# Optimization experiments

Hardware: AMD Instinct MI355X
Metric: run time of the kernel (lower is better)

The kernel has to match this reference:

```python
import jax, jax.numpy as jnp
import numpy as np


def setup_inputs() -> dict:
    key = jax.random.key(0)
    ks = jax.random.split(key, 7)
    C = 512
    x = jax.random.normal(ks[0], (16, C, 64, 64), dtype=jnp.float32)
    wq = jax.random.normal(ks[1], (C, C), dtype=jnp.float32) * (1.0 / np.sqrt(C))
    bq = jax.random.normal(ks[2], (C,), dtype=jnp.float32) * 0.02
    wk = jax.random.normal(ks[3], (C, C), dtype=jnp.float32) * (1.0 / np.sqrt(C))
    bk = jax.random.normal(ks[4], (C,), dtype=jnp.float32) * 0.02
    wo = jax.random.normal(ks[5], (C, C), dtype=jnp.float32) * (1.0 / np.sqrt(C))
    bo = jax.random.normal(ks[6], (C,), dtype=jnp.float32) * 0.02
    return {"x": x, "wq": wq, "bq": bq, "wk": wk, "bk": bk, "wo": wo, "bo": bo, "num_heads": 8}


def _conv1x1(x, w, b):
    # 1x1 conv == per-pixel linear map over channels; w: [Cout, Cin]
    return jnp.einsum('oc,bchw->bohw', w, x) + b[None, :, None, None]


def reference(x, wq, bq, wk, bk, wo, bo, num_heads):
    B, C, H, W = x.shape
    dh = C // num_heads
    P = H * W  # spatial positions (tokens)
    q = _conv1x1(x, wq, bq).reshape(B, num_heads, dh, P)
    k = _conv1x1(x, wk, bk).reshape(B, num_heads, dh, P)
    v = x.reshape(B, num_heads, dh, P)
    # NOTE: faithful to the torch code, attention is [B, nh, dh, dh]
    # (channel-channel scores contracted over spatial positions).
    att = jnp.einsum('bndp,bnep->bnde', q, k) / jnp.sqrt(jnp.asarray(dh, x.dtype))
    att = jax.nn.softmax(att, axis=-1)
    out = jnp.einsum('bnde,bnep->bndp', att, v).reshape(B, C, H, W)
    out = _conv1x1(out, wo, bo)
    return out + x
```

## Files before the change

### kernel.cpp

```cpp
#include <hip/hip_runtime.h>


typedef unsigned short ushort_t;
typedef __attribute__((ext_vector_type(8))) short bf16x8;
typedef __attribute__((ext_vector_type(4))) float f32x4;
typedef __attribute__((ext_vector_type(4))) unsigned short us4;
typedef __attribute__((ext_vector_type(8))) unsigned short us8;

#define NB 16
#define NC 512
#define NP 4096
#define NHD 8
#define DH 64

#define BM 128
#define BN 128
#define BKK 64

__device__ inline ushort_t f2bf(float f) {
  unsigned int u = __float_as_uint(f);
  u += 0x7FFFu + ((u >> 16) & 1u);
  return (ushort_t)(u >> 16);
}
__device__ inline float bf2f(ushort_t h) {
  return __uint_as_float(((unsigned int)h) << 16);
}

__device__ inline void gld_lds16(const void* g, void* l) {
  __builtin_amdgcn_global_load_lds(
      (const __attribute__((address_space(1))) unsigned int*)g,
      (__attribute__((address_space(3))) unsigned int*)l, 16, 0, 0);
}

__global__ __launch_bounds__(256, 4) void k_mfma_bt(
    const ushort_t* __restrict__ A, const ushort_t* __restrict__ B,
    void* __restrict__ Cv, const float* __restrict__ bias,
    int lda, int ldb, int ldc, long long sA, long long sB, long long sC,
    int Kper, int mode, int flags) {
  __shared__ __align__(128) ushort_t As[BM * BKK];
  __shared__ __align__(128) ushort_t Bs[BN * BKK];
  int m0, n0;
  long long zc;
  const ushort_t *Ab, *Bb;
  if (flags & 2) {
    int flat = blockIdx.x + 10 * blockIdx.z;
    int nf = (flat & 7) * 80 + (flat >> 3);
    int z2 = nf / 10, tile = nf - z2 * 10;
    int bb = z2 >> 2, sp = z2 & 3;
    int tm = (0x1A449000u >> (tile * 3)) & 7;
    int tn = (0x1B4D1688u >> (tile * 3)) & 7;
    m0 = tm * BM; n0 = tn * BN;
    Ab = A + bb * sA + (long long)sp * Kper;
    Bb = B + bb * sB + (long long)sp * Kper;
    zc = (long long)z2 * sC;
  } else {
    int bx = blockIdx.x, by = blockIdx.y;
    if (flags & 1) {
      int nxy = gridDim.x * gridDim.y;
      int id = bx + gridDim.x * by;
      int nid = (id & 7) * (nxy >> 3) + (id >> 3);
      bx = nid % gridDim.x; by = nid / gridDim.x;
    }
    m0 = by * BM; n0 = bx * BN;
    Ab = A + blockIdx.z * sA;
    Bb = B + blockIdx.z * sB;
    zc = (long long)blockIdx.z * sC;
  }
  int t = threadIdx.x;
  int lane = t & 63, w = t >> 6;
  int wr = w >> 1, wc = w & 1;
  int l15 = lane & 15, l4 = lane >> 4;
  int sr = lane >> 3, scc = lane & 7;

  f32x4 zero = {0.f, 0.f, 0.f, 0.f};
  f32x4 acc[4][4];
#pragma unroll
  for (int i = 0; i < 4; ++i)
#pragma unroll
    for (int j = 0; j < 4; ++j) acc[i][j] = zero;

  for (int k0 = 0; k0 < Kper; k0 += BKK) {
#pragma unroll
    for (int i = 0; i < 4; ++i) {
      int slab = w * 4 + i;
      int r = slab * 8 + sr;
      int kc = scc ^ (r & 7);
      gld_lds16(Ab + (size_t)(m0 + r) * lda + k0 + kc * 8, &As[slab * 512]);
      gld_lds16(Bb + (size_t)(n0 + r) * ldb + k0 + kc * 8, &Bs[slab * 512]);
    }
    __syncthreads();
#pragma unroll
    for (int kf = 0; kf < 2; ++kf) {
      bf16x8 av[4], bv[4];
#pragma unroll
      for (int i = 0; i < 4; ++i) {
        int r = wr * 64 + i * 16 + l15;
        int c = (kf * 4 + l4) ^ (r & 7);
        av[i] = *(const bf16x8*)&As[r * 64 + c * 8];
        int rn = wc * 64 + i * 16 + l15;
        int cn = (kf * 4 + l4) ^ (rn & 7);
        bv[i] = *(const bf16x8*)&Bs[rn * 64 + cn * 8];
      }
#pragma unroll
      for (int i = 0; i < 4; ++i)
#pragma unroll
        for (int j = 0; j < 4; ++j)
          acc[i][j] = __builtin_amdgcn_mfma_f32_16x16x32_bf16(av[i], bv[j],
                                                              acc[i][j], 0, 0, 0);
    }
    __syncthreads();
  }

  if (mode == 3) {
    ushort_t* C = (ushort_t*)Cv + zc;
#pragma unroll
    for (int i = 0; i < 4; ++i)
#pragma unroll
      for (int j = 0; j < 4; ++j)
#pragma unroll
        for (int rr = 0; rr < 4; ++rr) {
          int grow = m0 + wr * 64 + i * 16 + l4 * 4 + rr;
          int gcol = n0 + wc * 64 + j * 16 + l15;
          float v = acc[i][j][rr];
          ushort_t hi = f2bf(v);
          C[(size_t)grow * ldc + gcol] = hi;
          C[4194304 + (size_t)grow * ldc + gcol] = f2bf(v - bf2f(hi));
        }
  } else if (mode == 1) {
    float* C = (float*)Cv + zc;
#pragma unroll
    for (int i = 0; i < 4; ++i)
#pragma unroll
      for (int j = 0; j < 4; ++j)
#pragma unroll
        for (int rr = 0; rr < 4; ++rr) {
          int grow = m0 + wr * 64 + i * 16 + l4 * 4 + rr;
          int gcol = n0 + wc * 64 + j * 16 + l15;
          __builtin_nontemporal_store(acc[i][j][rr] + bias[grow],
                                      &C[(size_t)grow * ldc + gcol]);
        }
  } else {
    float* C = (float*)Cv + zc;
#pragma unroll
    for (int i = 0; i < 4; ++i)
#pragma unroll
      for (int j = 0; j < 4; ++j)
#pragma unroll
        for (int rr = 0; rr < 4; ++rr) {
          int grow = m0 + wr * 64 + i * 16 + l4 * 4 + rr;
          int gcol = n0 + wc * 64 + j * 16 + l15;
          C[(size_t)grow * ldc + gcol] = acc[i][j][rr];
        }
  }
}

__global__ __launch_bounds__(256) void k_prep(const float* __restrict__ x,
                                              ushort_t* __restrict__ xbf,
                                              ushort_t* __restrict__ xt,
                                              float* __restrict__ sPart) {
  __shared__ float tile[64][65];
  int b = blockIdx.z;
  const float* xb = x + (size_t)b * NC * NP;
  int t = threadIdx.x;
  int pp0 = blockIdx.x * 64, cc0 = blockIdx.y * 64;
#pragma unroll
  for (int i = 0; i < 4; ++i) {
    int idx = i * 256 + t;
    int r = idx >> 4, q = idx & 15;
    float4 v = *reinterpret_cast<const float4*>(
        xb + (size_t)(cc0 + r) * NP + pp0 + q * 4);
    us4 u = {f2bf(v.x), f2bf(v.y), f2bf(v.z), f2bf(v.w)};
    *reinterpret_cast<us4*>(
        &xbf[((size_t)b * NC + cc0 + r) * NP + pp0 + q * 4]) = u;
    tile[r][q * 4 + 0] = v.x; tile[r][q * 4 + 1] = v.y;
    tile[r][q * 4 + 2] = v.z; tile[r][q * 4 + 3] = v.w;
  }
  __syncthreads();
  {
    int r = t >> 2, q = t & 3;
    float ps = 0.f;
#pragma unroll
    for (int i = 0; i < 16; ++i) ps += tile[r][q * 16 + i];
    ps += __shfl_down(ps, 1, 64);
    ps += __shfl_down(ps, 2, 64);
    if (q == 0)
      sPart[(size_t)blockIdx.x * (NB * NC) + b * NC + cc0 + r] = ps;
  }
  {
    int p = t >> 2, cg = t & 3;
    us8 lo, hi;
#pragma unroll
    for (int i = 0; i < 8; ++i) lo[i] = f2bf(tile[cg * 16 + i][p]);
#pragma unroll
    for (int i = 0; i < 8; ++i) hi[i] = f2bf(tile[cg * 16 + 8 + i][p]);
    ushort_t* dst = &xt[((size_t)b * NP + pp0 + p) * NC + cc0 + cg * 16];
    *reinterpret_cast<us8*>(dst) = lo;
    *reinterpret_cast<us8*>(dst + 8) = hi;
  }
}

__global__ __launch_bounds__(256) void k_sreduce(const float* __restrict__ sPart,
                                                 float* __restrict__ s) {
  int idx = blockIdx.x * 256 + threadIdx.x;
  float a = 0.f;
  for (int pb = 0; pb < 64; ++pb) a += sPart[(size_t)pb * (NB * NC) + idx];
  s[idx] = a;
}

__global__ __launch_bounds__(256) void k_cvtw(
    const float* __restrict__ wq, const float* __restrict__ wk,
    const float* __restrict__ wo, ushort_t* __restrict__ q,
    ushort_t* __restrict__ k, ushort_t* __restrict__ o) {
  int i = blockIdx.x * 256 + threadIdx.x;
  q[i] = f2bf(wq[i]);
  k[i] = f2bf(wk[i]);
  o[i] = f2bf(wo[i]);
}

__global__ __launch_bounds__(256) void k_reduceG(const float* __restrict__ Gp,
                                                 ushort_t* __restrict__ Gb) {
  size_t i = (size_t)blockIdx.x * 256 + threadIdx.x;
  size_t b = i >> 18, idx = i & 262143;
  int r = (int)(idx >> 9), c = (int)(idx & 511);
  int rr = r, cc = c;
  if ((r >> 7) > (c >> 7)) { rr = c; cc = r; }
  const float* p = Gp + (b * 4) * 262144 + (size_t)rr * 512 + cc;
  float v = (p[0] + p[262144]) + (p[2 * 262144] + p[3 * 262144]);
  Gb[i] = f2bf(v);
}

__global__ __launch_bounds__(256) void k_uw(
    const float* __restrict__ wq, const float* __restrict__ wk,
    const float* __restrict__ s, float* __restrict__ U, float* __restrict__ W) {
  int b = blockIdx.x >> 3, n = blockIdx.x & 7;
  int t = threadIdx.x;
  __shared__ float ssh[NC];
  for (int i = t; i < NC; i += 256) ssh[i] = s[b * NC + i];
  __syncthreads();
  int pair = t >> 1, half = t & 1;
  int d = pair & 63, sel = pair >> 6;
  const float* row = (sel ? wk : wq) + (size_t)(n * DH + d) * NC + half * 256;
  const float* sb = ssh + half * 256;
  float a = 0.f;
#pragma unroll 8
  for (int i = 0; i < 64; ++i) {
    float4 v = reinterpret_cast<const float4*>(row)[i];
    a += v.x * sb[i * 4] + v.y * sb[i * 4 + 1] + v.z * sb[i * 4 + 2] +
         v.w * sb[i * 4 + 3];
  }
  a += __shfl_xor(a, 1, 64);
  if (half == 0) (sel ? W : U)[b * NC + n * DH + d] = a;
}

__global__ __launch_bounds__(256) void k_fused(
    const ushort_t* __restrict__ Thi, const ushort_t* __restrict__ Tlo,
    const ushort_t* __restrict__ Wkb, const ushort_t* __restrict__ Wob,
    const float* __restrict__ U, const float* __restrict__ Wv,
    const float* __restrict__ bq, const float* __restrict__ bk,
    ushort_t* __restrict__ Mb) {
  __shared__ __align__(128) ushort_t Th[64 * 64];
  __shared__ __align__(128) ushort_t Tl[64 * 64];
  __shared__ __align__(128) ushort_t Wks[64 * 64];
  __shared__ float Ps[64][65];
  __shared__ __align__(16) ushort_t PT[64 * 72];
  __shared__ __align__(128) ushort_t Wos[128 * 64];
  __shared__ float ush[64], wsh[64], bqs[64], bks[64];

  int b = blockIdx.x >> 4, n = (blockIdx.x >> 1) & 7, half = blockIdx.x & 1;
  int t = threadIdx.x, lane = t & 63, w = t >> 6;
  int l15 = lane & 15, l4 = lane >> 4;

  if (t < 64) ush[t] = U[b * NC + n * DH + t];
  else if (t < 128) wsh[t - 64] = Wv[b * NC + n * DH + (t - 64)];
  else if (t < 192) bqs[t - 128] = bq[n * DH + (t - 128)];
  else bks[t - 192] = bk[n * DH + (t - 192)];

  const size_t tbase = ((size_t)b * NC + n * DH) * NC;
  f32x4 zero = {0.f, 0.f, 0.f, 0.f};
  f32x4 acc[4];
#pragma unroll
  for (int i = 0; i < 4; ++i) acc[i] = zero;

  for (int kc0 = 0; kc0 < NC; kc0 += 64) {
    __syncthreads();
#pragma unroll
    for (int i = 0; i < 6; ++i) {
      int slab = w * 6 + i;
      int mat = slab >> 3, sl = slab & 7;
      int r = sl * 8 + (lane >> 3);
      int kc = (lane & 7) ^ (r & 7);
      if (mat == 0)
        gld_lds16(Thi + tbase + (size_t)r * NC + kc0 + kc * 8, &Th[sl * 512]);
      else if (mat == 1)
        gld_lds16(Tlo + tbase + (size_t)r * NC + kc0 + kc * 8, &Tl[sl * 512]);
      else
        gld_lds16(Wkb + (size_t)(n * DH + r) * NC + kc0 + kc * 8, &Wks[sl * 512]);
    }
    __syncthreads();
#pragma unroll
    for (int kf = 0; kf < 2; ++kf) {
      int rn = w * 16 + l15;
      int cn = (kf * 4 + l4) ^ (rn & 7);
      bf16x8 bvf = *(const bf16x8*)&Wks[rn * 64 + cn * 8];
#pragma unroll
      for (int i = 0; i < 4; ++i) {
        int r = i * 16 + l15;
        int c = (kf * 4 + l4) ^ (r & 7);
        bf16x8 ah = *(const bf16x8*)&Th[r * 64 + c * 8];
        bf16x8 al = *(const bf16x8*)&Tl[r * 64 + c * 8];
        acc[i] = __builtin_amdgcn_mfma_f32_16x16x32_bf16(ah, bvf, acc[i], 0, 0, 0);
        acc[i] = __builtin_amdgcn_mfma_f32_16x16x32_bf16(al, bvf, acc[i], 0, 0, 0);
      }
    }
  }
#pragma unroll
  for (int i = 0; i < 4; ++i)
#pragma unroll
    for (int rr = 0; rr < 4; ++rr) {
      int d = i * 16 + l4 * 4 + rr, e = w * 16 + l15;
      float v = acc[i][rr] + ush[d] * bks[e] + bqs[d] * (wsh[e] + 4096.f * bks[e]);
      Ps[d][e] = v * 0.125f;
    }
  __syncthreads();
  {
    int d = w * 16 + l15;
    float mx = -1e30f;
#pragma unroll
    for (int i = 0; i < 16; ++i) mx = fmaxf(mx, Ps[d][l4 * 16 + i]);
    mx = fmaxf(mx, __shfl_xor(mx, 16, 64));
    mx = fmaxf(mx, __shfl_xor(mx, 32, 64));
    float pv[16];
    float sum = 0.f;
#pragma unroll
    for (int i = 0; i < 16; ++i) {
      pv[i] = __expf(Ps[d][l4 * 16 + i] - mx);
      sum += pv[i];
    }
    sum += __shfl_xor(sum, 16, 64);
    sum += __shfl_xor(sum, 32, 64);
    float inv = 1.f / sum;
#pragma unroll
    for (int i = 0; i < 16; ++i) PT[(l4 * 16 + i) * 72 + d] = f2bf(pv[i] * inv);
  }
  for (int mi = 0; mi < 2; ++mi) {
    int mt = half * 2 + mi;
    __syncthreads();
#pragma unroll
    for (int i = 0; i < 4; ++i) {
      int slab = w * 4 + i;
      int r = slab * 8 + (lane >> 3);
      int kc = (lane & 7) ^ (r & 7);
      gld_lds16(Wob + (size_t)(mt * 128 + r) * NC + n * DH + kc * 8,
                &Wos[slab * 512]);
    }
    __syncthreads();
    f32x4 acc2[2][4];
#pragma unroll
    for (int i2 = 0; i2 < 2; ++i2)
#pragma unroll
      for (int j = 0; j < 4; ++j) acc2[i2][j] = zero;
#pragma unroll
    for (int kf = 0; kf < 2; ++kf) {
      bf16x8 bv[4];
#pragma unroll
      for (int j = 0; j < 4; ++j) {
        int e = j * 16 + l15;
        bv[j] = *(const bf16x8*)&PT[e * 72 + (kf * 4 + l4) * 8];
      }
#pragma unroll
      for (int i2 = 0; i2 < 2; ++i2) {
        int r = w * 32 + i2 * 16 + l15;
        int c = (kf * 4 + l4) ^ (r & 7);
        bf16x8 av = *(const bf16x8*)&Wos[r * 64 + c * 8];
#pragma unroll
        for (int j = 0; j < 4; ++j)
          acc2[i2][j] =
              __builtin_amdgcn_mfma_f32_16x16x32_bf16(av, bv[j], acc2[i2][j], 0, 0, 0);
      }
    }
#pragma unroll
    for (int i2 = 0; i2 < 2; ++i2)
#pragma unroll
      for (int j = 0; j < 4; ++j)
#pragma unroll
        for (int rr = 0; rr < 4; ++rr) {
          int grow = mt * 128 + w * 32 + i2 * 16 + l4 * 4 + rr;
          int gcol = n * DH + j * 16 + l15;
          float v = acc2[i2][j][rr];
          if (grow == gcol) v += 1.f;
          Mb[((size_t)b * NC + grow) * NC + gcol] = f2bf(v);
        }
  }
}

#define BKt 32
#define BMt 128
#define BNt 128
#define LDTK 132

__global__ __launch_bounds__(256) void k_rowsum(const float* __restrict__ x,
                                                float* __restrict__ s) {
  int row = blockIdx.x;
  const float* xr = x + (size_t)row * NP;
  int t = threadIdx.x;
  float acc = 0.f;
  for (int i = t; i < NP / 4; i += 256) {
    float4 v = reinterpret_cast<const float4*>(xr)[i];
    acc += (v.x + v.y) + (v.z + v.w);
  }
  for (int off = 32; off > 0; off >>= 1) acc += __shfl_down(acc, off, 64);
  __shared__ float red[4];
  int lane = t & 63, wv = t >> 6;
  if (lane == 0) red[wv] = acc;
  __syncthreads();
  if (t == 0) s[row] = (red[0] + red[1]) + (red[2] + red[3]);
}

__global__ __launch_bounds__(256) void k_gemm_abT(
    const float* __restrict__ Abase, const float* __restrict__ Bbase,
    float* __restrict__ Cbase, int K, int lda, int ldb, int ldc,
    size_t sA, size_t sB, size_t sC) {
  __shared__ float As[BKt][LDTK];
  __shared__ float Bs[BKt][LDTK];
  const float* A = Abase + sA * blockIdx.z;
  const float* Bm = Bbase + sB * blockIdx.z;
  float* Cm = Cbase + sC * blockIdx.z;
  int m0 = blockIdx.y * BMt, n0 = blockIdx.x * BNt;
  int t = threadIdx.x;
  int tr = t >> 4, tc = t & 15;
  float acc[8][8];
#pragma unroll
  for (int i = 0; i < 8; ++i)
#pragma unroll
    for (int j = 0; j < 8; ++j) acc[i][j] = 0.f;
  for (int k0 = 0; k0 < K; k0 += BKt) {
#pragma unroll
    for (int it = 0; it < 4; ++it) {
      int idx = it * 256 + t;
      int r = idx >> 3, kq = idx & 7;
      float4 va = *reinterpret_cast<const float4*>(A + (size_t)(m0 + r) * lda + k0 + kq * 4);
      As[kq * 4 + 0][r] = va.x; As[kq * 4 + 1][r] = va.y;
      As[kq * 4 + 2][r] = va.z; As[kq * 4 + 3][r] = va.w;
      float4 vb = *reinterpret_cast<const float4*>(Bm + (size_t)(n0 + r) * ldb + k0 + kq * 4);
      Bs[kq * 4 + 0][r] = vb.x; Bs[kq * 4 + 1][r] = vb.y;
      Bs[kq * 4 + 2][r] = vb.z; Bs[kq * 4 + 3][r] = vb.w;
    }
    __syncthreads();
#pragma unroll
    for (int kk = 0; kk < BKt; ++kk) {
      float4 a0 = *reinterpret_cast<const float4*>(&As[kk][tr * 8]);
      float4 a1 = *reinterpret_cast<const float4*>(&As[kk][tr * 8 + 4]);
      float4 b0 = *reinterpret_cast<const float4*>(&Bs[kk][tc * 8]);
      float4 b1 = *reinterpret_cast<const float4*>(&Bs[kk][tc * 8 + 4]);
      float av[8] = {a0.x, a0.y, a0.z, a0.w, a1.x, a1.y, a1.z, a1.w};
      float bv[8] = {b0.x, b0.y, b0.z, b0.w, b1.x, b1.y, b1.z, b1.w};
#pragma unroll
      for (int i = 0; i < 8; ++i)
#pragma unroll
        for (int j = 0; j < 8; ++j) acc[i][j] += av[i] * bv[j];
    }
    __syncthreads();
  }
#pragma unroll
  for (int i = 0; i < 8; ++i) {
    float* crow = Cm + (size_t)(m0 + tr * 8 + i) * ldc + n0 + tc * 8;
    float4 c0 = {acc[i][0], acc[i][1], acc[i][2], acc[i][3]};
    float4 c1 = {acc[i][4], acc[i][5], acc[i][6], acc[i][7]};
    *reinterpret_cast<float4*>(crow) = c0;
    *reinterpret_cast<float4*>(crow + 4) = c1;
  }
}

__global__ __launch_bounds__(256) void k_gemm_ab(
    const float* __restrict__ Abase, const float* __restrict__ Bbase,
    float* __restrict__ Cbase, const float* __restrict__ bias,
    int K, int lda, int ldb, int ldc, size_t sA, size_t sB, size_t sC) {
  __shared__ float As[BKt][LDTK];
  __shared__ float Bs[BKt][LDTK];
  const float* A = Abase + sA * blockIdx.z;
  const float* Bm = Bbase + sB * blockIdx.z;
  float* Cm = Cbase + sC * blockIdx.z;
  int m0 = blockIdx.y * BMt, n0 = blockIdx.x * BNt;
  int t = threadIdx.x;
  int tr = t >> 4, tc = t & 15;
  float acc[8][8];
#pragma unroll
  for (int i = 0; i < 8; ++i)
#pragma unroll
    for (int j = 0; j < 8; ++j) acc[i][j] = 0.f;
  for (int k0 = 0; k0 < K; k0 += BKt) {
#pragma unroll
    for (int it = 0; it < 4; ++it) {
      int idx = it * 256 + t;
      int r = idx >> 3, kq = idx & 7;
      float4 va = *reinterpret_cast<const float4*>(A + (size_t)(m0 + r) * lda + k0 + kq * 4);
      As[kq * 4 + 0][r] = va.x; As[kq * 4 + 1][r] = va.y;
      As[kq * 4 + 2][r] = va.z; As[kq * 4 + 3][r] = va.w;
      int kk = idx >> 5, nq = idx & 31;
      float4 vb = *reinterpret_cast<const float4*>(Bm + (size_t)(k0 + kk) * ldb + n0 + nq * 4);
      *reinterpret_cast<float4*>(&Bs[kk][nq * 4]) = vb;
    }
    __syncthreads();
#pragma unroll
    for (int kk = 0; kk < BKt; ++kk) {
      float4 a0 = *reinterpret_cast<const float4*>(&As[kk][tr * 8]);
      float4 a1 = *reinterpret_cast<const float4*>(&As[kk][tr * 8 + 4]);
      float4 b0 = *reinterpret_cast<const float4*>(&Bs[kk][tc * 8]);
      float4 b1 = *reinterpret_cast<const float4*>(&Bs[kk][tc * 8 + 4]);
      float av[8] = {a0.x, a0.y, a0.z, a0.w, a1.x, a1.y, a1.z, a1.w};
      float bv[8] = {b0.x, b0.y, b0.z, b0.w, b1.x, b1.y, b1.z, b1.w};
#pragma unroll
      for (int i = 0; i < 8; ++i)
#pragma unroll
        for (int j = 0; j < 8; ++j) acc[i][j] += av[i] * bv[j];
    }
    __syncthreads();
  }
#pragma unroll
  for (int i = 0; i < 8; ++i) {
    int row = m0 + tr * 8 + i;
    float bb = bias ? bias[row] : 0.f;
    float* crow = Cm + (size_t)row * ldc + n0 + tc * 8;
    float4 c0 = {acc[i][0] + bb, acc[i][1] + bb, acc[i][2] + bb, acc[i][3] + bb};
    float4 c1 = {acc[i][4] + bb, acc[i][5] + bb, acc[i][6] + bb, acc[i][7] + bb};
    *reinterpret_cast<float4*>(crow) = c0;
    *reinterpret_cast<float4*>(crow + 4) = c1;
  }
}

__global__ __launch_bounds__(256) void k_att(
    const float* __restrict__ T, const float* __restrict__ wq,
    const float* __restrict__ bq, const float* __restrict__ wk,
    const float* __restrict__ bk, const float* __restrict__ wo,
    const float* __restrict__ s, float* __restrict__ Mf) {
  int b = blockIdx.x >> 3, n = blockIdx.x & 7;
  int t = threadIdx.x;
  __shared__ float sh_s[NC];
  __shared__ float sh_u[DH], sh_w[DH];
  __shared__ float L[DH][DH + 1];
  __shared__ float Ts[DH][68];
  __shared__ float Ks[DH][68];

  for (int i = t; i < NC; i += 256) sh_s[i] = s[b * NC + i];
  __syncthreads();
  if (t < 128) {
    int d = t & 63;
    const float* wrow = (t < 64 ? wq : wk) + (size_t)(n * DH + d) * NC;
    float a = 0.f;
    for (int c = 0; c < NC; ++c) a += wrow[c] * sh_s[c];
    if (t < 64) sh_u[d] = a; else sh_w[d] = a;
  }

  int d = t >> 2, eg = t & 3;
  float acc[16];
#pragma unroll
  for (int i = 0; i < 16; ++i) acc[i] = 0.f;

  for (int c0 = 0; c0 < NC; c0 += 64) {
#pragma unroll
    for (int it = 0; it < 4; ++it) {
      int idx = it * 256 + t;
      int r = idx >> 4, cq = idx & 15;
      float4 v = *reinterpret_cast<const float4*>(
          T + ((size_t)b * NC + n * DH + r) * NC + c0 + cq * 4);
      *reinterpret_cast<float4*>(&Ts[r][cq * 4]) = v;
      float4 kv = *reinterpret_cast<const float4*>(
          wk + (size_t)(n * DH + r) * NC + c0 + cq * 4);
      Ks[cq * 4 + 0][r] = kv.x; Ks[cq * 4 + 1][r] = kv.y;
      Ks[cq * 4 + 2][r] = kv.z; Ks[cq * 4 + 3][r] = kv.w;
    }
    __syncthreads();
    for (int cc = 0; cc < 64; ++cc) {
      float tv = Ts[d][cc];
      float4 k0v = *reinterpret_cast<const float4*>(&Ks[cc][eg * 16]);
      float4 k1v = *reinterpret_cast<const float4*>(&Ks[cc][eg * 16 + 4]);
      float4 k2v = *reinterpret_cast<const float4*>(&Ks[cc][eg * 16 + 8]);
      float4 k3v = *reinterpret_cast<const float4*>(&Ks[cc][eg * 16 + 12]);
      acc[0] += tv * k0v.x;  acc[1] += tv * k0v.y;
      acc[2] += tv * k0v.z;  acc[3] += tv * k0v.w;
      acc[4] += tv * k1v.x;  acc[5] += tv * k1v.y;
      acc[6] += tv * k1v.z;  acc[7] += tv * k1v.w;
      acc[8] += tv * k2v.x;  acc[9] += tv * k2v.y;
      acc[10] += tv * k2v.z; acc[11] += tv * k2v.w;
      acc[12] += tv * k3v.x; acc[13] += tv * k3v.y;
      acc[14] += tv * k3v.z; acc[15] += tv * k3v.w;
    }
    __syncthreads();
  }

  float bqd = bq[n * DH + d];
  float ud = sh_u[d];
#pragma unroll
  for (int i = 0; i < 16; ++i) {
    int e = eg * 16 + i;
    float bke = bk[n * DH + e];
    L[d][e] = (acc[i] + ud * bke + bqd * (sh_w[e] + (float)NP * bke)) * 0.125f;
  }
  __syncthreads();
  if (t < 64) {
    float mx = -1e30f;
    for (int e = 0; e < DH; ++e) mx = fmaxf(mx, L[t][e]);
    float sum = 0.f;
    for (int e = 0; e < DH; ++e) { float p = __expf(L[t][e] - mx); L[t][e] = p; sum += p; }
    float inv = 1.f / sum;
    for (int e = 0; e < DH; ++e) L[t][e] *= inv;
  }
  __syncthreads();

#pragma unroll
  for (int rep = 0; rep < 2; ++rep) {
    int o = rep * 256 + t;
    const float* worow = wo + (size_t)o * NC + n * DH;
    float wreg[64];
#pragma unroll
    for (int q = 0; q < 16; ++q) {
      float4 v = *reinterpret_cast<const float4*>(worow + q * 4);
      wreg[q * 4 + 0] = v.x; wreg[q * 4 + 1] = v.y;
      wreg[q * 4 + 2] = v.z; wreg[q * 4 + 3] = v.w;
    }
    for (int e = 0; e < DH; ++e) {
      float a = 0.f;
#pragma unroll
      for (int dd = 0; dd < DH; ++dd) a += wreg[dd] * L[dd][e];
      int col = n * DH + e;
      if (o == col) a += 1.f;
      Mf[((size_t)b * NC + o) * NC + col] = a;
    }
  }
}

extern "C" void kernel_launch(void* const* d_in, const int* in_sizes, int n_in,
                              void* d_out, int out_size, void* d_ws, size_t ws_size,
                              hipStream_t stream) {
  const float* x  = (const float*)d_in[0];
  const float* wq = (const float*)d_in[1];
  const float* bq = (const float*)d_in[2];
  const float* wk = (const float*)d_in[3];
  const float* bk = (const float*)d_in[4];
  const float* wo = (const float*)d_in[5];
  const float* bo = (const float*)d_in[6];
  float* out = (float*)d_out;
  char* ws = (char*)d_ws;

  const size_t sX = (size_t)NC * NP;
  const size_t sG = (size_t)NC * NC;
  const size_t xbf_bytes = (size_t)NB * sX * 2;

  size_t off_s  = 0;
  size_t off_sp = 32768;
  size_t off_xt = off_sp + (size_t)64 * NB * NC * 4;
  size_t off_mb = off_xt + xbf_bytes;
  size_t off_wq = off_mb + (size_t)NB * sG * 2;
  size_t off_wk = off_wq + sG * 2;
  size_t off_wo = off_wk + sG * 2;
  size_t off_u  = off_wo + sG * 2;
  size_t off_w  = off_u + 32768;
  size_t need   = off_w + 32768;

  if (ws_size >= need + 4096) {
    float*    s     = (float*)(ws + off_s);
    float*    sPart = (float*)(ws + off_sp);
    ushort_t* Xt    = (ushort_t*)(ws + off_xt);
    ushort_t* Mb    = (ushort_t*)(ws + off_mb);
    ushort_t* Wqb   = (ushort_t*)(ws + off_wq);
    ushort_t* Wkb   = (ushort_t*)(ws + off_wk);
    ushort_t* Wob   = (ushort_t*)(ws + off_wo);
    float*    U     = (float*)(ws + off_u);
    float*    W     = (float*)(ws + off_w);
    char* dob = (char*)d_out;
    ushort_t* Xbf   = (ushort_t*)d_out;
    float*    Gpart = (float*)(dob + xbf_bytes);
    ushort_t* Gb    = (ushort_t*)d_out;
    ushort_t* Thi   = (ushort_t*)(dob + xbf_bytes);
    ushort_t* Tlo   = Thi + 4194304;

    k_cvtw<<<dim3(1024), 256, 0, stream>>>(wq, wk, wo, Wqb, Wkb, Wob);
    k_prep<<<dim3(64, 8, 16), 256, 0, stream>>>(x, Xbf, Xt, sPart);
    k_sreduce<<<dim3(32), 256, 0, stream>>>(sPart, s);
    k_uw<<<dim3(NB * NHD), 256, 0, stream>>>(wq, wk, s, U, W);
    k_mfma_bt<<<dim3(10, 1, 64), 256, 0, stream>>>(
        Xbf, Xbf, Gpart, nullptr, NP, NP, NC,
        (long long)sX, (long long)sX, (long long)sG, NP / 4, 2, 2);
    k_reduceG<<<16384, 256, 0, stream>>>(Gpart, Gb);
    k_mfma_bt<<<dim3(4, 4, 16), 256, 0, stream>>>(
        Wqb, Gb, Thi, nullptr, NC, NC, NC,
        0LL, (long long)sG, (long long)sG, NC, 3, 1);
    k_fused<<<dim3(NB * NHD * 2), 256, 0, stream>>>(Thi, Tlo, Wkb, Wob, U, W,
                                                    bq, bk, Mb);
    k_mfma_bt<<<dim3(32, 4, 16), 256, 0, stream>>>(
        Mb, Xt, out, bo, NC, NC, NP,
        (long long)sG, (long long)sX, (long long)sX, NC, 1, 1);
  } else {
    float* s  = (float*)ws;
    float* G  = (float*)(ws + 32768);
    float* Tm = (float*)(ws + 32768 + (size_t)NB * sG * 4);
    float* M  = G;
    k_rowsum<<<NB * NC, 256, 0, stream>>>(x, s);
    k_gemm_abT<<<dim3(4, 4, NB), 256, 0, stream>>>(x, x, G, NP, NP, NP, NC, sX, sX, sG);
    k_gemm_ab<<<dim3(4, 4, NB), 256, 0, stream>>>(wq, G, Tm, nullptr, NC, NC, NC, NC,
                                                  0, sG, sG);
    k_att<<<NB * NHD, 256, 0, stream>>>(Tm, wq, bq, wk, bk, wo, s, M);
    k_gemm_ab<<<dim3(NP / BNt, NC / BMt, NB), 256, 0, stream>>>(M, x, out, bo, NC, NC,
                                                                NP, NP, sG, sX, sX);
  }
}
```

Baseline: 241.1 us.

## Stage GEMM epilogue through LDS and coalesce prep and Gram-reduce kernels

The GEMM epilogue now writes each accumulator tile into shared memory in two halves and stores it back as row-contiguous float4 vectors, with bias folded in, instead of scattered scalar stores. The prep kernel moves to 128x128 tiles, reduces row sums with warp shuffles, and transposes through a bf16 LDS tile. The Gram reduction only reads the computed upper-triangle tiles with vector loads and writes the mirrored tile through an LDS transpose. These changes target uncoalesced global traffic, at the cost of extra barriers and more LDS per block.

```diff
diff --git a/kernel.cpp b/kernel.cpp
--- a/kernel.cpp
+++ b/kernel.cpp
@@ -37,8 +37,9 @@
     void* __restrict__ Cv, const float* __restrict__ bias,
     int lda, int ldb, int ldc, long long sA, long long sB, long long sC,
     int Kper, int mode, int flags) {
-  __shared__ __align__(128) ushort_t As[BM * BKK];
-  __shared__ __align__(128) ushort_t Bs[BN * BKK];
+  __shared__ __align__(128) ushort_t Smem[16640];
+  ushort_t* As = Smem;
+  ushort_t* Bs = Smem + 8320;
   int m0, n0;
   long long zc;
   const ushort_t *Ab, *Bb;
@@ -126,31 +127,39 @@
           C[(size_t)grow * ldc + gcol] = hi;
           C[4194304 + (size_t)grow * ldc + gcol] = f2bf(v - bf2f(hi));
         }
-  } else if (mode == 1) {
-    float* C = (float*)Cv + zc;
-#pragma unroll
-    for (int i = 0; i < 4; ++i)
-#pragma unroll
-      for (int j = 0; j < 4; ++j)
-#pragma unroll
-        for (int rr = 0; rr < 4; ++rr) {
-          int grow = m0 + wr * 64 + i * 16 + l4 * 4 + rr;
-          int gcol = n0 + wc * 64 + j * 16 + l15;
-          __builtin_nontemporal_store(acc[i][j][rr] + bias[grow],
-                                      &C[(size_t)grow * ldc + gcol]);
-        }
   } else {
     float* C = (float*)Cv + zc;
-#pragma unroll
-    for (int i = 0; i < 4; ++i)
-#pragma unroll
-      for (int j = 0; j < 4; ++j)
-#pragma unroll
-        for (int rr = 0; rr < 4; ++rr) {
-          int grow = m0 + wr * 64 + i * 16 + l4 * 4 + rr;
-          int gcol = n0 + wc * 64 + j * 16 + l15;
-          C[(size_t)grow * ldc + gcol] = acc[i][j][rr];
+    float* fbuf = (float*)Smem;
+#pragma unroll
+    for (int ch = 0; ch < 2; ++ch) {
+      if (wr == ch) {
+#pragma unroll
+        for (int i = 0; i < 4; ++i)
+#pragma unroll
+          for (int j = 0; j < 4; ++j)
+#pragma unroll
+            for (int rr = 0; rr < 4; ++rr)
+              fbuf[(i * 16 + l4 * 4 + rr) * 130 + wc * 64 + j * 16 + l15] =
+                  acc[i][j][rr];
+      }
+      __syncthreads();
+      {
+        int row = t >> 2, q = t & 3;
+        int grow = m0 + ch * 64 + row;
+        float bb = (mode == 1) ? bias[grow] : 0.f;
+        float* crow = C + (size_t)grow * ldc + n0 + q * 32;
+#pragma unroll
+        for (int u = 0; u < 8; ++u) {
+          f32x4 v = *reinterpret_cast<const f32x4*>(&fbuf[row * 130 + q * 32 + u * 4]);
+          v[0] += bb; v[1] += bb; v[2] += bb; v[3] += bb;
+          if (mode == 1)
+            __builtin_nontemporal_store(v, reinterpret_cast<f32x4*>(crow + u * 4));
+          else
+            *reinterpret_cast<f32x4*>(crow + u * 4) = v;
         }
+      }
+      __syncthreads();
+    }
   }
 }
 
@@ -158,44 +167,37 @@
                                               ushort_t* __restrict__ xbf,
                                               ushort_t* __restrict__ xt,
                                               float* __restrict__ sPart) {
-  __shared__ float tile[64][65];
+  __shared__ ushort_t ldsC[128 * 132];
   int b = blockIdx.z;
-  const float* xb = x + (size_t)b * NC * NP;
+  int pp0 = blockIdx.x * 128, cc0 = blockIdx.y * 128;
+  const float* xb = x + ((size_t)b * NC + cc0) * NP + pp0;
   int t = threadIdx.x;
-  int pp0 = blockIdx.x * 64, cc0 = blockIdx.y * 64;
-#pragma unroll
-  for (int i = 0; i < 4; ++i) {
-    int idx = i * 256 + t;
-    int r = idx >> 4, q = idx & 15;
-    float4 v = *reinterpret_cast<const float4*>(
-        xb + (size_t)(cc0 + r) * NP + pp0 + q * 4);
+  int rq = t >> 5;
+  int q  = t & 31;
+#pragma unroll
+  for (int i = 0; i < 16; ++i) {
+    int r = i * 8 + rq;
+    float4 v = *reinterpret_cast<const float4*>(xb + (size_t)r * NP + q * 4);
     us4 u = {f2bf(v.x), f2bf(v.y), f2bf(v.z), f2bf(v.w)};
-    *reinterpret_cast<us4*>(
-        &xbf[((size_t)b * NC + cc0 + r) * NP + pp0 + q * 4]) = u;
-    tile[r][q * 4 + 0] = v.x; tile[r][q * 4 + 1] = v.y;
-    tile[r][q * 4 + 2] = v.z; tile[r][q * 4 + 3] = v.w;
+    *reinterpret_cast<us4*>(&xbf[((size_t)b * NC + cc0 + r) * NP + pp0 + q * 4]) = u;
+    *reinterpret_cast<us4*>(&ldsC[r * 132 + q * 4]) = u;
+    float s4 = (v.x + v.y) + (v.z + v.w);
+    s4 += __shfl_xor(s4, 1, 32);
+    s4 += __shfl_xor(s4, 2, 32);
+    s4 += __shfl_xor(s4, 4, 32);
+    s4 += __shfl_xor(s4, 8, 32);
+    s4 += __shfl_xor(s4, 16, 32);
+    if (q == 0) sPart[(size_t)blockIdx.x * (NB * NC) + b * NC + cc0 + r] = s4;
   }
   __syncthreads();
-  {
-    int r = t >> 2, q = t & 3;
-    float ps = 0.f;
-#pragma unroll
-    for (int i = 0; i < 16; ++i) ps += tile[r][q * 16 + i];
-    ps += __shfl_down(ps, 1, 64);
-    ps += __shfl_down(ps, 2, 64);
-    if (q == 0)
-      sPart[(size_t)blockIdx.x * (NB * NC) + b * NC + cc0 + r] = ps;
-  }
-  {
-    int p = t >> 2, cg = t & 3;
-    us8 lo, hi;
-#pragma unroll
-    for (int i = 0; i < 8; ++i) lo[i] = f2bf(tile[cg * 16 + i][p]);
-#pragma unroll
-    for (int i = 0; i < 8; ++i) hi[i] = f2bf(tile[cg * 16 + 8 + i][p]);
-    ushort_t* dst = &xt[((size_t)b * NP + pp0 + p) * NC + cc0 + cg * 16];
-    *reinterpret_cast<us8*>(dst) = lo;
-    *reinterpret_cast<us8*>(dst + 8) = hi;
+  int p = t >> 1, chalf = (t & 1) * 64;
+  ushort_t* dst = &xt[((size_t)b * NP + pp0 + p) * NC + cc0 + chalf];
+#pragma unroll
+  for (int g = 0; g < 8; ++g) {
+    us8 o;
+#pragma unroll
+    for (int j = 0; j < 8; ++j) o[j] = ldsC[(chalf + g * 8 + j) * 132 + p];
+    *reinterpret_cast<us8*>(dst + g * 8) = o;
   }
 }
 
@@ -203,7 +205,7 @@
                                                  float* __restrict__ s) {
   int idx = blockIdx.x * 256 + threadIdx.x;
   float a = 0.f;
-  for (int pb = 0; pb < 64; ++pb) a += sPart[(size_t)pb * (NB * NC) + idx];
+  for (int pb = 0; pb < 32; ++pb) a += sPart[(size_t)pb * (NB * NC) + idx];
   s[idx] = a;
 }
 
@@ -219,14 +221,42 @@
 
 __global__ __launch_bounds__(256) void k_reduceG(const float* __restrict__ Gp,
                                                  ushort_t* __restrict__ Gb) {
-  size_t i = (size_t)blockIdx.x * 256 + threadIdx.x;
-  size_t b = i >> 18, idx = i & 262143;
-  int r = (int)(idx >> 9), c = (int)(idx & 511);
-  int rr = r, cc = c;
-  if ((r >> 7) > (c >> 7)) { rr = c; cc = r; }
-  const float* p = Gp + (b * 4) * 262144 + (size_t)rr * 512 + cc;
-  float v = (p[0] + p[262144]) + (p[2 * 262144] + p[3 * 262144]);
-  Gb[i] = f2bf(v);
+  __shared__ ushort_t ldsM[128 * 36];
+  int slab = blockIdx.x, tile = blockIdx.y, b = blockIdx.z;
+  int tm = (0x1A449000u >> (tile * 3)) & 7;
+  int tn = (0x1B4D1688u >> (tile * 3)) & 7;
+  int t = threadIdx.x;
+  const float* base = Gp + ((size_t)b * 4) * 262144 +
+                      (size_t)(tm * 128) * 512 + tn * 128 + slab * 32;
+  ushort_t* gb = Gb + (size_t)b * 262144;
+#pragma unroll
+  for (int i = 0; i < 4; ++i) {
+    int idx = i * 256 + t;
+    int r = idx >> 3, lq = idx & 7;
+    const float* p = base + (size_t)r * 512 + lq * 4;
+    float4 v0 = *reinterpret_cast<const float4*>(p);
+    float4 v1 = *reinterpret_cast<const float4*>(p + 262144);
+    float4 v2 = *reinterpret_cast<const float4*>(p + 2 * 262144);
+    float4 v3 = *reinterpret_cast<const float4*>(p + 3 * 262144);
+    us4 u = {f2bf((v0.x + v1.x) + (v2.x + v3.x)),
+             f2bf((v0.y + v1.y) + (v2.y + v3.y)),
+             f2bf((v0.z + v1.z) + (v2.z + v3.z)),
+             f2bf((v0.w + v1.w) + (v2.w + v3.w))};
+    *reinterpret_cast<us4*>(
+        &gb[(size_t)(tm * 128 + r) * 512 + tn * 128 + slab * 32 + lq * 4]) = u;
+    if (tm != tn) *reinterpret_cast<us4*>(&ldsM[r * 36 + lq * 4]) = u;
+  }
+  if (tm == tn) return;
+  __syncthreads();
+  int orow = t >> 3, og = t & 7;
+  ushort_t* dst = &gb[(size_t)(tn * 128 + slab * 32 + orow) * 512 + tm * 128 + og * 16];
+#pragma unroll
+  for (int h = 0; h < 2; ++h) {
+    us8 o;
+#pragma unroll
+    for (int j = 0; j < 8; ++j) o[j] = ldsM[(og * 16 + h * 8 + j) * 36 + orow];
+    *reinterpret_cast<us8*>(dst + h * 8) = o;
+  }
 }
 
 __global__ __launch_bounds__(256) void k_uw(
@@ -675,13 +705,13 @@
     ushort_t* Tlo   = Thi + 4194304;
 
     k_cvtw<<<dim3(1024), 256, 0, stream>>>(wq, wk, wo, Wqb, Wkb, Wob);
-    k_prep<<<dim3(64, 8, 16), 256, 0, stream>>>(x, Xbf, Xt, sPart);
+    k_prep<<<dim3(32, 4, 16), 256, 0, stream>>>(x, Xbf, Xt, sPart);
     k_sreduce<<<dim3(32), 256, 0, stream>>>(sPart, s);
     k_uw<<<dim3(NB * NHD), 256, 0, stream>>>(wq, wk, s, U, W);
     k_mfma_bt<<<dim3(10, 1, 64), 256, 0, stream>>>(
         Xbf, Xbf, Gpart, nullptr, NP, NP, NC,
         (long long)sX, (long long)sX, (long long)sG, NP / 4, 2, 2);
-    k_reduceG<<<16384, 256, 0, stream>>>(Gpart, Gb);
+    k_reduceG<<<dim3(4, 10, 16), 256, 0, stream>>>(Gpart, Gb);
     k_mfma_bt<<<dim3(4, 4, 16), 256, 0, stream>>>(
         Wqb, Gb, Thi, nullptr, NC, NC, NC,
         0LL, (long long)sG, (long long)sG, NC, 3, 1);
```

New measurement: 236.1 us. -2.0%, faster.
